# Kernel tuning notes

Hardware: AMD Instinct MI355X
Metric: run time of the kernel (lower is better)

## Reference

```python
import jax, jax.numpy as jnp
import numpy as np

N = 50000
E = 640000
D_IN = 128
D_OUT = 128


def setup_inputs() -> dict:
    key = jax.random.key(0)
    k1, k2, k3, k4 = jax.random.split(key, 4)
    x = jax.random.normal(k1, (N, D_IN), dtype=jnp.float32)
    edge_index = jax.random.randint(k2, (2, E), 0, N, dtype=jnp.int64)
    # Linear(in_channels, out_channels) params, PyTorch default init scale
    lim = 1.0 / np.sqrt(D_IN)
    W = jax.random.uniform(k3, (D_IN, D_OUT), dtype=jnp.float32, minval=-lim, maxval=lim)
    b = jax.random.uniform(k4, (D_OUT,), dtype=jnp.float32, minval=-lim, maxval=lim)
    return {"x": x, "edge_index": edge_index, "W": W, "b": b}


def reference(x, edge_index, W, b):
    row, col = edge_index[0], edge_index[1]
    # gather source features, segment-sum onto destination rows
    msgs = x[col]  # [E, D_IN]
    summed = jax.ops.segment_sum(msgs, row, num_segments=N)  # [N, D_IN]
    counts = jax.ops.segment_sum(jnp.ones((E,), dtype=x.dtype), row, num_segments=N)
    # scatter_mean: empty segments -> 0 (avoid div by zero)
    x_agg = summed / jnp.maximum(counts, 1.0)[:, None]
    # Linear + ReLU
    return jax.nn.relu(x_agg @ W + b)
```

## Files before the change

### kernel.cpp

```cpp
#include <hip/hip_runtime.h>

#define NN 50000
#define DD 128
#define PAD 16
#define CAP 48
#define GEMM_BLOCKS 391

typedef __attribute__((ext_vector_type(8))) short bf16x8;
typedef __attribute__((ext_vector_type(4))) float f32x4;

static __device__ __forceinline__ unsigned short f2bf(float x) {
    unsigned int u = __float_as_uint(x);
    unsigned int r = (u + 0x7fffu + ((u >> 16) & 1u)) >> 16;
    return (unsigned short)r;
}

static __device__ __forceinline__ int swz(int byte) {
    return byte ^ (((byte >> 8) & 7) << 4);
}

__global__ void __launch_bounds__(512) gemm_xw_kernel(
    const float* __restrict__ x,
    const float* __restrict__ W,
    unsigned short* __restrict__ y,
    int* __restrict__ pad)
{
    __shared__ unsigned short w_lds[DD * DD];
    __shared__ unsigned short r_lds[128 * DD];

    const int tid = threadIdx.x;
    const int i0 = blockIdx.x * 128;

    {
        int gid = blockIdx.x * 512 + tid;
        if (gid < NN * PAD / 4) {
            reinterpret_cast<uint4*>(pad)[gid] = make_uint4(0u, 0u, 0u, 0u);
        }
    }

    {
        const int j = tid & 127;
        #pragma unroll
        for (int it = 0; it < 8; ++it) {
            int kbase = (tid >> 7) * 4 + it * 16;
            float v0 = W[(kbase + 0) * DD + j];
            float v1 = W[(kbase + 1) * DD + j];
            float v2 = W[(kbase + 2) * DD + j];
            float v3 = W[(kbase + 3) * DD + j];
            ushort4 o;
            o.x = f2bf(v0); o.y = f2bf(v1); o.z = f2bf(v2); o.w = f2bf(v3);
            *reinterpret_cast<ushort4*>((char*)w_lds + swz(j * 256 + kbase * 2)) = o;
        }
    }

    const int wave = tid >> 6;
    const int l64 = tid & 63;
    const int lrow = l64 & 15;
    const int kgrp = l64 >> 4;
    const int grow = min(i0 + wave * 16 + lrow, NN - 1);

    bf16x8 afrag[4];
    #pragma unroll
    for (int s = 0; s < 4; ++s) {
        const float4* xp = reinterpret_cast<const float4*>(
            x + (size_t)grow * DD + s * 32 + kgrp * 8);
        float4 p0 = xp[0];
        float4 p1 = xp[1];
        bf16x8 a;
        a[0] = (short)f2bf(p0.x); a[1] = (short)f2bf(p0.y);
        a[2] = (short)f2bf(p0.z); a[3] = (short)f2bf(p0.w);
        a[4] = (short)f2bf(p1.x); a[5] = (short)f2bf(p1.y);
        a[6] = (short)f2bf(p1.z); a[7] = (short)f2bf(p1.w);
        afrag[s] = a;
    }
    __syncthreads();

    f32x4 acc[8];
    #pragma unroll
    for (int t = 0; t < 8; ++t) acc[t] = (f32x4){0.f, 0.f, 0.f, 0.f};

    #pragma unroll
    for (int t = 0; t < 8; ++t) {
        #pragma unroll
        for (int s = 0; s < 4; ++s) {
            int byte = (t * 16 + lrow) * 256 + (s * 32 + kgrp * 8) * 2;
            bf16x8 bfrag = *reinterpret_cast<const bf16x8*>((char*)w_lds + swz(byte));
            acc[t] = __builtin_amdgcn_mfma_f32_16x16x32_bf16(afrag[s], bfrag, acc[t], 0, 0, 0);
        }
    }

    #pragma unroll
    for (int t = 0; t < 8; ++t) {
        #pragma unroll
        for (int r = 0; r < 4; ++r) {
            int lr = wave * 16 + kgrp * 4 + r;
            int byte = lr * 256 + (t * 16 + lrow) * 2;
            *reinterpret_cast<unsigned short*>((char*)r_lds + swz(byte)) = f2bf(acc[t][r]);
        }
    }
    __syncthreads();

    {
        uint4* dst = reinterpret_cast<uint4*>(y) + (size_t)i0 * 16;
        #pragma unroll
        for (int it = 0; it < 4; ++it) {
            int idx = tid + it * 512;
            if (i0 + (idx >> 4) < NN) {
                uint4 v = *reinterpret_cast<const uint4*>((char*)r_lds + swz(idx * 16));
                dst[idx] = v;
            }
        }
    }
}

__global__ void __launch_bounds__(256) ticket_place_kernel(
    const int* __restrict__ row, const int* __restrict__ col,
    int* __restrict__ pad, unsigned short* __restrict__ slot, int E)
{
    int e = blockIdx.x * 256 + threadIdx.x;
    if (e < E) {
        int r = row[e];
        int t = atomicAdd(&pad[r * PAD], 1);
        if (t < CAP) slot[r * CAP + t] = (unsigned short)col[e];
    }
}

__global__ void __launch_bounds__(256) gather_out_kernel(
    const unsigned short* __restrict__ y,
    const int* __restrict__ pad,
    const unsigned short* __restrict__ slot,
    const float* __restrict__ bias,
    float* __restrict__ out)
{
    int node = blockIdx.x * 8 + (threadIdx.x >> 5);
    int lane = threadIdx.x & 31;
    int q = lane >> 3;
    int l8 = lane & 7;
    if (node >= NN) return;
    int cnt0 = pad[node * PAD];
    int cnt = min(cnt0, CAP);
    int start = node * CAP;
    int end = start + cnt;

    float acc[16];
    #pragma unroll
    for (int j = 0; j < 16; ++j) acc[j] = 0.f;

    for (int base = start; base < end; base += 32) {
        int cl = (base + lane < end) ? (int)slot[base + lane] : 0;
        int m = min(32, end - base);
        for (int ii = 0; ii < m; ii += 4) {
            int src = ii + q;
            int c = __shfl(cl, src, 32);
            if (src < m) {
                const uint4* yp = reinterpret_cast<const uint4*>(y + (size_t)c * DD) + 2 * l8;
                uint4 u0 = yp[0];
                uint4 u1 = yp[1];
                acc[0]  += __uint_as_float(u0.x << 16);
                acc[1]  += __uint_as_float(u0.x & 0xffff0000u);
                acc[2]  += __uint_as_float(u0.y << 16);
                acc[3]  += __uint_as_float(u0.y & 0xffff0000u);
                acc[4]  += __uint_as_float(u0.z << 16);
                acc[5]  += __uint_as_float(u0.z & 0xffff0000u);
                acc[6]  += __uint_as_float(u0.w << 16);
                acc[7]  += __uint_as_float(u0.w & 0xffff0000u);
                acc[8]  += __uint_as_float(u1.x << 16);
                acc[9]  += __uint_as_float(u1.x & 0xffff0000u);
                acc[10] += __uint_as_float(u1.y << 16);
                acc[11] += __uint_as_float(u1.y & 0xffff0000u);
                acc[12] += __uint_as_float(u1.z << 16);
                acc[13] += __uint_as_float(u1.z & 0xffff0000u);
                acc[14] += __uint_as_float(u1.w << 16);
                acc[15] += __uint_as_float(u1.w & 0xffff0000u);
            }
        }
    }
    #pragma unroll
    for (int j = 0; j < 16; ++j) {
        acc[j] += __shfl_xor(acc[j], 8, 32);
        acc[j] += __shfl_xor(acc[j], 16, 32);
    }

    float inv = 1.0f / fmaxf((float)cnt0, 1.0f);
    float4 bb = reinterpret_cast<const float4*>(bias)[4 * l8 + q];
    float4 o;
    o.x = fmaxf(acc[4 * q + 0] * inv + bb.x, 0.f);
    o.y = fmaxf(acc[4 * q + 1] * inv + bb.y, 0.f);
    o.z = fmaxf(acc[4 * q + 2] * inv + bb.z, 0.f);
    o.w = fmaxf(acc[4 * q + 3] * inv + bb.w, 0.f);
    reinterpret_cast<float4*>(out + (size_t)node * DD)[4 * l8 + q] = o;
}

__global__ void __launch_bounds__(256) wt_only_kernel(
    const float* __restrict__ W, unsigned short* __restrict__ Wt)
{
    for (int idx = threadIdx.x; idx < DD * DD; idx += 256) {
        int k = idx >> 7;
        int j = idx & 127;
        Wt[j * DD + k] = f2bf(W[idx]);
    }
}

__global__ void __launch_bounds__(256) scatter_atomic_kernel(
    const float* __restrict__ x,
    const int* __restrict__ row, const int* __restrict__ col,
    float* __restrict__ agg, int* __restrict__ counts, int E)
{
    int gid = blockIdx.x * blockDim.x + threadIdx.x;
    int group = gid >> 5;
    int lane = threadIdx.x & 31;
    int ngroups = (gridDim.x * blockDim.x) >> 5;
    for (int e = group; e < E; e += ngroups) {
        int r = row[e];
        int c = col[e];
        float4 v = reinterpret_cast<const float4*>(x + (size_t)c * DD)[lane];
        float* dst = agg + (size_t)r * DD + lane * 4;
        unsafeAtomicAdd(dst + 0, v.x);
        unsafeAtomicAdd(dst + 1, v.y);
        unsafeAtomicAdd(dst + 2, v.z);
        unsafeAtomicAdd(dst + 3, v.w);
        if (lane == 0) atomicAdd(counts + r, 1);
    }
}

__global__ void __launch_bounds__(256) gemm_fb_kernel(
    const float* __restrict__ agg,
    const int* __restrict__ counts,
    const unsigned short* __restrict__ Wt,
    const float* __restrict__ bias,
    float* __restrict__ out)
{
    __shared__ unsigned short w_lds[DD * DD];
    __shared__ unsigned short a_lds[64 * DD];
    __shared__ float b_lds[DD];

    const int tid = threadIdx.x;
    const int i0 = blockIdx.x * 64;

    {
        const uint4* src = reinterpret_cast<const uint4*>(Wt);
        #pragma unroll
        for (int it = 0; it < 8; ++it) {
            int idx = tid + it * 256;
            *reinterpret_cast<uint4*>((char*)w_lds + swz(idx * 16)) = src[idx];
        }
    }
    if (tid < DD) b_lds[tid] = bias[tid];

    #pragma unroll
    for (int it = 0; it < 8; ++it) {
        int idx = tid + it * 256;
        int r = idx >> 5;
        int c4 = idx & 31;
        int grow = i0 + r;
        float4 v = make_float4(0.f, 0.f, 0.f, 0.f);
        float inv = 0.f;
        if (grow < NN) {
            v = reinterpret_cast<const float4*>(agg + (size_t)grow * DD)[c4];
            inv = 1.0f / fmaxf((float)counts[grow], 1.0f);
        }
        ushort4 o;
        o.x = f2bf(v.x * inv); o.y = f2bf(v.y * inv);
        o.z = f2bf(v.z * inv); o.w = f2bf(v.w * inv);
        *reinterpret_cast<ushort4*>((char*)a_lds + swz(r * 256 + c4 * 8)) = o;
    }
    __syncthreads();

    const int wave = tid >> 6;
    const int l64 = tid & 63;
    const int lrow = l64 & 15;
    const int kgrp = l64 >> 4;

    bf16x8 afrag[4];
    #pragma unroll
    for (int s = 0; s < 4; ++s) {
        int byte = (wave * 16 + lrow) * 256 + (s * 32 + kgrp * 8) * 2;
        afrag[s] = *reinterpret_cast<const bf16x8*>((char*)a_lds + swz(byte));
    }

    f32x4 acc[8];
    #pragma unroll
    for (int t = 0; t < 8; ++t) acc[t] = (f32x4){0.f, 0.f, 0.f, 0.f};

    #pragma unroll
    for (int t = 0; t < 8; ++t) {
        #pragma unroll
        for (int s = 0; s < 4; ++s) {
            int byte = (t * 16 + lrow) * 256 + (s * 32 + kgrp * 8) * 2;
            bf16x8 bfrag = *reinterpret_cast<const bf16x8*>((char*)w_lds + swz(byte));
            acc[t] = __builtin_amdgcn_mfma_f32_16x16x32_bf16(afrag[s], bfrag, acc[t], 0, 0, 0);
        }
    }

    #pragma unroll
    for (int t = 0; t < 8; ++t) {
        int colj = t * 16 + lrow;
        float bbv = b_lds[colj];
        #pragma unroll
        for (int r = 0; r < 4; ++r) {
            int grow = i0 + wave * 16 + kgrp * 4 + r;
            if (grow < NN) {
                out[(size_t)grow * DD + colj] = fmaxf(acc[t][r] + bbv, 0.f);
            }
        }
    }
}

extern "C" void kernel_launch(void* const* d_in, const int* in_sizes, int n_in,
                              void* d_out, int out_size, void* d_ws, size_t ws_size,
                              hipStream_t stream) {
    const float* x  = (const float*)d_in[0];
    const int* ei   = (const int*)d_in[1];
    const float* W  = (const float*)d_in[2];
    const float* b  = (const float*)d_in[3];
    float* out      = (float*)d_out;

    const int E = in_sizes[1] / 2;
    const int* row = ei;
    const int* col = ei + E;

    char* wsc = (char*)d_ws;
    int* pad             = (int*)(wsc + 0);
    unsigned short* slot = (unsigned short*)(wsc + 3200000);
    unsigned short* y    = (unsigned short*)(wsc + 8000000);
    const size_t WS_NEED = 20800000;

    const int EB = (E + 255) / 256;

    if (ws_size >= WS_NEED) {
        gemm_xw_kernel<<<GEMM_BLOCKS, 512, 0, stream>>>(x, W, y, pad);
        ticket_place_kernel<<<EB, 256, 0, stream>>>(row, col, pad, slot, E);
        gather_out_kernel<<<(NN + 7) / 8, 256, 0, stream>>>(y, pad, slot, b, out);
    } else {
        int* fc = (int*)d_ws;
        unsigned short* fWt = (unsigned short*)(wsc + 200704);
        hipMemsetAsync(d_out, 0, (size_t)NN * DD * sizeof(float), stream);
        hipMemsetAsync(fc, 0, (size_t)NN * sizeof(int), stream);
        wt_only_kernel<<<1, 256, 0, stream>>>(W, fWt);
        scatter_atomic_kernel<<<2048, 256, 0, stream>>>(x, row, col, out, fc, E);
        gemm_fb_kernel<<<(NN + 63) / 64, 256, 0, stream>>>(out, fc, fWt, b, out);
    }
}
```

Before: 76.95 us.

## Fuse GEMM, edge bucketing and gather into one cooperative persistent kernel

Replaces the three-kernel sequence with a single cooperative-launch kernel that uses grid syncs. About two thirds of the blocks run the bf16 MFMA X·W GEMM while the rest bucket edges into per-node slots at the same time, and after a grid sync all blocks do the mean-gather plus bias and ReLU. This is meant to remove launch gaps and to overlap the GEMM with the atomic edge placement. In exchange it pays for two grid-wide barriers, reloads W into LDS for every extra tile, and falls back to the old path if the cooperative launch fails.

```diff
diff --git a/kernel.cpp b/kernel.cpp
--- a/kernel.cpp
+++ b/kernel.cpp
@@ -1,9 +1,13 @@
 #include <hip/hip_runtime.h>
+#include <hip/hip_cooperative_groups.h>
+
+namespace cg = cooperative_groups;
 
 #define NN 50000
 #define DD 128
 #define PAD 16
 #define CAP 48
+#define NTILES 782
 #define GEMM_BLOCKS 391
 
 typedef __attribute__((ext_vector_type(8))) short bf16x8;
@@ -18,6 +22,195 @@
 static __device__ __forceinline__ int swz(int byte) {
     return byte ^ (((byte >> 8) & 7) << 4);
 }
+
+__global__ void __launch_bounds__(256) fused_kernel(
+    const float* __restrict__ x,
+    const float* __restrict__ W,
+    const int* __restrict__ row, const int* __restrict__ col,
+    const float* __restrict__ bias,
+    int* __restrict__ pad, unsigned short* __restrict__ slot,
+    unsigned short* __restrict__ y, float* __restrict__ out, int E)
+{
+    __shared__ unsigned short w_lds[DD * DD];
+
+    const int tid = threadIdx.x;
+    const int bid = blockIdx.x;
+    const int grid = gridDim.x;
+    const int gG = min(NTILES, (grid * 2) / 3);
+    const bool is_gemm = (bid < gG);
+
+    {
+        int stride = grid * 256;
+        for (int i = bid * 256 + tid; i < NN * PAD / 4; i += stride)
+            reinterpret_cast<uint4*>(pad)[i] = make_uint4(0u, 0u, 0u, 0u);
+    }
+    if (is_gemm) {
+        const int j = tid & 127;
+        #pragma unroll
+        for (int it = 0; it < 16; ++it) {
+            int kbase = (tid >> 7) * 4 + it * 8;
+            float v0 = W[(kbase + 0) * DD + j];
+            float v1 = W[(kbase + 1) * DD + j];
+            float v2 = W[(kbase + 2) * DD + j];
+            float v3 = W[(kbase + 3) * DD + j];
+            ushort4 o;
+            o.x = f2bf(v0); o.y = f2bf(v1); o.z = f2bf(v2); o.w = f2bf(v3);
+            *reinterpret_cast<ushort4*>((char*)w_lds + swz(j * 256 + kbase * 2)) = o;
+        }
+    }
+    __threadfence();
+    cg::this_grid().sync();
+
+    if (is_gemm) {
+        const int wave = tid >> 6;
+        const int l64 = tid & 63;
+        const int lrow = l64 & 15;
+        const int kgrp = l64 >> 4;
+
+        for (int tile = bid; tile < NTILES; tile += gG) {
+            if (tile != bid) {
+                __syncthreads();
+                const int j = tid & 127;
+                #pragma unroll
+                for (int it = 0; it < 16; ++it) {
+                    int kbase = (tid >> 7) * 4 + it * 8;
+                    float v0 = W[(kbase + 0) * DD + j];
+                    float v1 = W[(kbase + 1) * DD + j];
+                    float v2 = W[(kbase + 2) * DD + j];
+                    float v3 = W[(kbase + 3) * DD + j];
+                    ushort4 o;
+                    o.x = f2bf(v0); o.y = f2bf(v1); o.z = f2bf(v2); o.w = f2bf(v3);
+                    *reinterpret_cast<ushort4*>((char*)w_lds + swz(j * 256 + kbase * 2)) = o;
+                }
+                __syncthreads();
+            }
+            const int i0 = tile * 64;
+            const int grow = min(i0 + wave * 16 + lrow, NN - 1);
+
+            bf16x8 afrag[4];
+            #pragma unroll
+            for (int s = 0; s < 4; ++s) {
+                const float4* xp = reinterpret_cast<const float4*>(
+                    x + (size_t)grow * DD + s * 32 + kgrp * 8);
+                float4 p0 = xp[0];
+                float4 p1 = xp[1];
+                bf16x8 a;
+                a[0] = (short)f2bf(p0.x); a[1] = (short)f2bf(p0.y);
+                a[2] = (short)f2bf(p0.z); a[3] = (short)f2bf(p0.w);
+                a[4] = (short)f2bf(p1.x); a[5] = (short)f2bf(p1.y);
+                a[6] = (short)f2bf(p1.z); a[7] = (short)f2bf(p1.w);
+                afrag[s] = a;
+            }
+
+            f32x4 acc[8];
+            #pragma unroll
+            for (int t = 0; t < 8; ++t) acc[t] = (f32x4){0.f, 0.f, 0.f, 0.f};
+
+            #pragma unroll
+            for (int t = 0; t < 8; ++t) {
+                #pragma unroll
+                for (int s = 0; s < 4; ++s) {
+                    int byte = (t * 16 + lrow) * 256 + (s * 32 + kgrp * 8) * 2;
+                    bf16x8 bfrag = *reinterpret_cast<const bf16x8*>((char*)w_lds + swz(byte));
+                    acc[t] = __builtin_amdgcn_mfma_f32_16x16x32_bf16(afrag[s], bfrag, acc[t], 0, 0, 0);
+                }
+            }
+            __syncthreads();
+
+            #pragma unroll
+            for (int t = 0; t < 8; ++t) {
+                #pragma unroll
+                for (int r = 0; r < 4; ++r) {
+                    int lr = wave * 16 + kgrp * 4 + r;
+                    int byte = lr * 256 + (t * 16 + lrow) * 2;
+                    *reinterpret_cast<unsigned short*>((char*)w_lds + swz(byte)) = f2bf(acc[t][r]);
+                }
+            }
+            __syncthreads();
+
+            uint4* dst = reinterpret_cast<uint4*>(y) + (size_t)i0 * 16;
+            #pragma unroll
+            for (int it = 0; it < 4; ++it) {
+                int idx = tid + it * 256;
+                if (i0 + (idx >> 4) < NN) {
+                    uint4 v = *reinterpret_cast<const uint4*>((char*)w_lds + swz(idx * 16));
+                    dst[idx] = v;
+                }
+            }
+        }
+    } else {
+        const int tb = grid - gG;
+        for (int e = (bid - gG) * 256 + tid; e < E; e += tb * 256) {
+            int r = row[e];
+            int t = atomicAdd(&pad[r * PAD], 1);
+            if (t < CAP) slot[r * CAP + t] = (unsigned short)col[e];
+        }
+    }
+    __threadfence();
+    cg::this_grid().sync();
+
+    const int lane = tid & 31;
+    const int q = lane >> 3;
+    const int l8 = lane & 7;
+    for (int nb = bid * 8; nb < NN; nb += grid * 8) {
+        int node = nb + (tid >> 5);
+        if (node < NN) {
+            int cnt0 = pad[node * PAD];
+            int cnt = min(cnt0, CAP);
+            int start = node * CAP;
+            int end = start + cnt;
+
+            float acc[16];
+            #pragma unroll
+            for (int j = 0; j < 16; ++j) acc[j] = 0.f;
+
+            for (int base = start; base < end; base += 32) {
+                int cl = (base + lane < end) ? (int)slot[base + lane] : 0;
+                int m = min(32, end - base);
+                for (int ii = 0; ii < m; ii += 4) {
+                    int src = ii + q;
+                    int c = __shfl(cl, src, 32);
+                    if (src < m) {
+                        const uint4* yp = reinterpret_cast<const uint4*>(y + (size_t)c * DD) + 2 * l8;
+                        uint4 u0 = yp[0];
+                        uint4 u1 = yp[1];
+                        acc[0]  += __uint_as_float(u0.x << 16);
+                        acc[1]  += __uint_as_float(u0.x & 0xffff0000u);
+                        acc[2]  += __uint_as_float(u0.y << 16);
+                        acc[3]  += __uint_as_float(u0.y & 0xffff0000u);
+                        acc[4]  += __uint_as_float(u0.z << 16);
+                        acc[5]  += __uint_as_float(u0.z & 0xffff0000u);
+                        acc[6]  += __uint_as_float(u0.w << 16);
+                        acc[7]  += __uint_as_float(u0.w & 0xffff0000u);
+                        acc[8]  += __uint_as_float(u1.x << 16);
+                        acc[9]  += __uint_as_float(u1.x & 0xffff0000u);
+                        acc[10] += __uint_as_float(u1.y << 16);
+                        acc[11] += __uint_as_float(u1.y & 0xffff0000u);
+                        acc[12] += __uint_as_float(u1.z << 16);
+                        acc[13] += __uint_as_float(u1.z & 0xffff0000u);
+                        acc[14] += __uint_as_float(u1.w << 16);
+                        acc[15] += __uint_as_float(u1.w & 0xffff0000u);
+                    }
+                }
+            }
+            #pragma unroll
+            for (int j = 0; j < 16; ++j) {
+                acc[j] += __shfl_xor(acc[j], 8, 32);
+                acc[j] += __shfl_xor(acc[j], 16, 32);
+            }
+
+            float inv = 1.0f / fmaxf((float)cnt0, 1.0f);
+            float4 bb = reinterpret_cast<const float4*>(bias)[4 * l8 + q];
+            float4 o;
+            o.x = fmaxf(acc[4 * q + 0] * inv + bb.x, 0.f);
+            o.y = fmaxf(acc[4 * q + 1] * inv + bb.y, 0.f);
+            o.z = fmaxf(acc[4 * q + 2] * inv + bb.z, 0.f);
+            o.w = fmaxf(acc[4 * q + 3] * inv + bb.w, 0.f);
+            reinterpret_cast<float4*>(out + (size_t)node * DD)[4 * l8 + q] = o;
+        }
+    }
+}
+
 
 __global__ void __launch_bounds__(512) gemm_xw_kernel(
     const float* __restrict__ x,
@@ -37,7 +230,6 @@
             reinterpret_cast<uint4*>(pad)[gid] = make_uint4(0u, 0u, 0u, 0u);
         }
     }
-
     {
         const int j = tid & 127;
         #pragma unroll
@@ -328,9 +520,25 @@
     const int EB = (E + 255) / 256;
 
     if (ws_size >= WS_NEED) {
-        gemm_xw_kernel<<<GEMM_BLOCKS, 512, 0, stream>>>(x, W, y, pad);
-        ticket_place_kernel<<<EB, 256, 0, stream>>>(row, col, pad, slot, E);
-        gather_out_kernel<<<(NN + 7) / 8, 256, 0, stream>>>(y, pad, slot, b, out);
+        int maxB = 0;
+        hipError_t qerr = hipOccupancyMaxActiveBlocksPerMultiprocessor(
+            &maxB, fused_kernel, 256, 0);
+        int grid = (qerr == hipSuccess && maxB >= 1) ? maxB * 256 : 0;
+        if (grid > 2048) grid = 2048;
+
+        hipError_t lerr = hipErrorUnknown;
+        if (grid >= 64) {
+            void* args[] = { (void*)&x, (void*)&W, (void*)&row, (void*)&col,
+                             (void*)&b, (void*)&pad, (void*)&slot, (void*)&y,
+                             (void*)&out, (void*)&E };
+            lerr = hipLaunchCooperativeKernel(fused_kernel, dim3(grid), dim3(256),
+                                              args, 0, stream);
+        }
+        if (lerr != hipSuccess) {
+            gemm_xw_kernel<<<GEMM_BLOCKS, 512, 0, stream>>>(x, W, y, pad);
+            ticket_place_kernel<<<EB, 256, 0, stream>>>(row, col, pad, slot, E);
+            gather_out_kernel<<<(NN + 7) / 8, 256, 0, stream>>>(y, pad, slot, b, out);
+        }
     } else {
         int* fc = (int*)d_ws;
         unsigned short* fWt = (unsigned short*)(wsc + 200704);
```

Result: slower. 245.4 us (+219.0%).
